# Kernel tuning notes

Hardware: AMD Instinct MI355X
Metric: run time of the kernel (lower is better)

Reference implementation:

```python
import jax, jax.numpy as jnp
import numpy as np

N_NODES = 50000
N_EDGES = 1600000
IN_CH = 128
HID_CH = 128


def setup_inputs() -> dict:
    key = jax.random.key(0)
    ks = jax.random.split(key, 8)
    node_embed = jax.random.normal(ks[0], (N_NODES, IN_CH), dtype=jnp.float32)
    node_pos = jax.random.normal(ks[1], (N_NODES, 3), dtype=jnp.float32)
    edge_index = jax.random.randint(ks[2], (2, N_EDGES), 0, N_NODES, dtype=jnp.int64)
    # Linear weights stored as [in, out] so y = x @ W + b (matches torch x @ W.T + b)
    W_res = jax.random.normal(ks[3], (IN_CH, HID_CH), dtype=jnp.float32) / np.sqrt(IN_CH)
    W_msg = jax.random.normal(ks[4], (2 * IN_CH + 1, HID_CH), dtype=jnp.float32) / np.sqrt(2 * IN_CH + 1)
    b_msg = jax.random.normal(ks[5], (HID_CH,), dtype=jnp.float32) * 0.01
    W_upd = jax.random.normal(ks[6], (IN_CH + HID_CH, HID_CH), dtype=jnp.float32) / np.sqrt(IN_CH + HID_CH)
    b_upd = jax.random.normal(ks[7], (HID_CH,), dtype=jnp.float32) * 0.01
    return {"node_embed": node_embed, "node_pos": node_pos, "edge_index": edge_index,
            "W_res": W_res, "W_msg": W_msg, "b_msg": b_msg, "W_upd": W_upd, "b_upd": b_upd}


def reference(node_embed, node_pos, edge_index, W_res, W_msg, b_msg, W_upd, b_upd):
    row, col = edge_index[0], edge_index[1]
    # squared distance per edge: [E, 1]
    diff = node_pos[row] - node_pos[col]
    dist = jnp.sum(diff * diff, axis=1, keepdims=True)
    # message MLP on concat(src, tgt, dist): [E, 2*in+1] -> [E, hidden]
    msg_in = jnp.concatenate([node_embed[row], node_embed[col], dist], axis=-1)
    msg = jax.nn.relu(msg_in @ W_msg + b_msg)
    # scatter-sum messages into target nodes (index = col, as in original)
    aggr = jax.ops.segment_sum(msg, col, num_segments=N_NODES)
    upd_in = jnp.concatenate([node_embed, aggr], axis=-1)
    new_node_embed = node_embed @ W_res + jax.nn.relu(upd_in @ W_upd + b_upd)
    return new_node_embed
```

## Files before the change

### kernel.cpp

```cpp
#include <hip/hip_runtime.h>
#include <hip/hip_bf16.h>
#include <cstdint>


typedef __bf16 bf16x8 __attribute__((ext_vector_type(8)));
typedef float floatx4 __attribute__((ext_vector_type(4)));
typedef float floatx2 __attribute__((ext_vector_type(2)));
typedef unsigned int uintx4 __attribute__((ext_vector_type(4)));

#define SBINS 128
#define SBIN_SHIFT 9
#define BIN_CAP 17408
#define CAP_OUT 19456
#define CUR_STRIDE 32

__device__ __forceinline__ ushort f2bf(float f) {
  union { float f; uint i; } v; v.f = f;
  uint r = v.i + 0x7fff + ((v.i >> 16) & 1);
  return (ushort)(r >> 16);
}
__device__ __forceinline__ bf16x8 load_frag(const ushort* p) {
  uint4 v = *(const uint4*)p;
  return __builtin_bit_cast(bf16x8, v);
}
__device__ __forceinline__ floatx2 pmax0(floatx2 a) {
#if __has_builtin(__builtin_elementwise_max)
  return __builtin_elementwise_max(a, (floatx2)(0.f));
#else
  floatx2 r; r.x = fmaxf(a.x, 0.f); r.y = fmaxf(a.y, 0.f); return r;
#endif
}
__device__ __forceinline__ floatx2 cvtpk2(uint qu) {
#if __has_builtin(__builtin_amdgcn_cvt_pk_f32_fp8)
  return __builtin_amdgcn_cvt_pk_f32_fp8((int)qu, false);
#else
  floatx2 o = {__builtin_amdgcn_cvt_f32_fp8((int)qu, 0),
               __builtin_amdgcn_cvt_f32_fp8((int)qu, 1)};
  return o;
#endif
}

struct WSrc { const float* s[5]; };

__global__ __launch_bounds__(256) void k01_cast_bin(
    const float* __restrict__ embed, ushort* __restrict__ Eb, int n4, int nb_cast,
    WSrc ws, ushort* __restrict__ Wt,
    const int* __restrict__ ei, int E,
    uint* __restrict__ bin_cursor, uint* __restrict__ binned, int bb)
{
  __shared__ uint hist[SBINS];
  __shared__ uint sbase[SBINS];
  __shared__ uint lcur[SBINS];

  if ((int)blockIdx.x >= bb) {
    int cb = blockIdx.x - bb;
    if (cb < nb_cast) {
      int i = cb * 256 + threadIdx.x;
      if (i < n4) {
        float4 v = ((const float4*)embed)[i];
        ushort4 o;
        o.x = f2bf(v.x); o.y = f2bf(v.y); o.z = f2bf(v.z); o.w = f2bf(v.w);
        ((ushort4*)Eb)[i] = o;
      }
      return;
    }
    int wb = cb - nb_cast;
    const float* s = ws.s[wb];
    ushort* d = Wt + wb * 16384;
    for (int i = threadIdx.x; i < 16384; i += 256) {
      int k = i >> 7, n = i & 127;
      d[n * 128 + k] = f2bf(s[i]);
    }
    return;
  }

  const int t = threadIdx.x;
  if (t < SBINS) hist[t] = 0;
  __syncthreads();

  const int e0 = blockIdx.x * 2048 + t * 8;
  int rr[8], cc[8];
  bool any = (e0 < E);
  if (any) {
    int4 r0 = ((const int4*)(ei + e0))[0];
    int4 r1 = ((const int4*)(ei + e0))[1];
    int4 c0 = ((const int4*)(ei + E + e0))[0];
    int4 c1 = ((const int4*)(ei + E + e0))[1];
    rr[0]=r0.x; rr[1]=r0.y; rr[2]=r0.z; rr[3]=r0.w;
    rr[4]=r1.x; rr[5]=r1.y; rr[6]=r1.z; rr[7]=r1.w;
    cc[0]=c0.x; cc[1]=c0.y; cc[2]=c0.z; cc[3]=c0.w;
    cc[4]=c1.x; cc[5]=c1.y; cc[6]=c1.z; cc[7]=c1.w;
#pragma unroll
    for (int j = 0; j < 8; ++j) {
      if (e0 + j < E) atomicAdd(&hist[cc[j] >> SBIN_SHIFT], 1u);
    }
  }
  __syncthreads();
  if (t < SBINS) {
    uint h = hist[t];
    sbase[t] = h ? atomicAdd(bin_cursor + t * CUR_STRIDE, h) : 0u;
    lcur[t] = 0;
  }
  __syncthreads();
  if (any) {
#pragma unroll
    for (int j = 0; j < 8; ++j) {
      if (e0 + j < E) {
        int b = cc[j] >> SBIN_SHIFT;
        uint ofs = atomicAdd(&lcur[b], 1u);
        uint idx = sbase[b] + ofs;
        if (idx < BIN_CAP)
          binned[(size_t)b * BIN_CAP + idx] = ((uint)cc[j] << 16) | (uint)rr[j];
      }
    }
  }
}

__global__ __launch_bounds__(256) void k2_proj_sort(
    const ushort* __restrict__ Ab, int M, int rt,
    const ushort* __restrict__ W1t, const ushort* __restrict__ W2t,
    const float* __restrict__ b_msg, const float* __restrict__ pos,
    unsigned char* __restrict__ P1, ushort* __restrict__ P2b,
    const uint* __restrict__ bin_cursor, const uint* __restrict__ binned,
    uint* __restrict__ sorted, int* __restrict__ nstart, int* __restrict__ ncnt)
{
  __shared__ uint  hist[512], st[512], lcur[512];
  __shared__ uint  part[256];
  __shared__ float spos[512 * 3];

  if ((int)blockIdx.x >= rt) {
    const int bin = blockIdx.x - rt;
    const int col0 = bin << SBIN_SHIFT;
    const int tid = threadIdx.x;
    const int cnt = (int)min(bin_cursor[bin * CUR_STRIDE], (uint)BIN_CAP);
    const uint* src = binned + (size_t)bin * BIN_CAP;
    const int ncol = min(512, M - col0);

    for (int i = tid; i < 512; i += 256) { hist[i] = 0; lcur[i] = 0; }
    for (int i = tid; i < ncol * 3; i += 256) spos[i] = pos[(size_t)col0 * 3 + i];
    __syncthreads();

    for (int i = tid; i < cnt; i += 256)
      atomicAdd(&hist[(src[i] >> 16) & 511u], 1u);
    __syncthreads();

    {
      uint a = hist[2 * tid], b = hist[2 * tid + 1];
      part[tid] = ((a + 3u) & ~3u) + ((b + 3u) & ~3u);
    }
    __syncthreads();
    if (tid == 0) {
      uint run = 0;
      for (int k = 0; k < 256; ++k) { uint tmp = part[k]; part[k] = run; run += tmp; }
    }
    __syncthreads();
    {
      uint a = hist[2 * tid];
      st[2 * tid] = part[tid];
      st[2 * tid + 1] = part[tid] + ((a + 3u) & ~3u);
    }
    __syncthreads();

    const size_t obase = (size_t)bin * CAP_OUT;
    int i = tid;
    for (; i + 1792 < cnt; i += 2048) {
      uint rc[8]; float dd[8];
#pragma unroll
      for (int j = 0; j < 8; ++j) rc[j] = src[i + j * 256];
#pragma unroll
      for (int j = 0; j < 8; ++j) {
        uint row = rc[j] & 0xffffu;
        uint cl  = (rc[j] >> 16) & 511u;
        float dx = spos[cl * 3 + 0] - pos[(size_t)row * 3 + 0];
        float dy = spos[cl * 3 + 1] - pos[(size_t)row * 3 + 1];
        float dz = spos[cl * 3 + 2] - pos[(size_t)row * 3 + 2];
        dd[j] = dx * dx + dy * dy + dz * dz;
      }
#pragma unroll
      for (int j = 0; j < 8; ++j) {
        uint cl = (rc[j] >> 16) & 511u;
        uint p = st[cl] + atomicAdd(&lcur[cl], 1u);
        sorted[obase + p] = (rc[j] << 16) | (uint)f2bf(dd[j]);
      }
    }
    for (; i < cnt; i += 256) {
      uint rc = src[i];
      uint row = rc & 0xffffu;
      uint cl  = (rc >> 16) & 511u;
      float dx = spos[cl * 3 + 0] - pos[(size_t)row * 3 + 0];
      float dy = spos[cl * 3 + 1] - pos[(size_t)row * 3 + 1];
      float dz = spos[cl * 3 + 2] - pos[(size_t)row * 3 + 2];
      float d = dx * dx + dy * dy + dz * dz;
      uint p = st[cl] + atomicAdd(&lcur[cl], 1u);
      sorted[obase + p] = (rc << 16) | (uint)f2bf(d);
    }
    __syncthreads();

    for (int c = tid; c < ncol; c += 256) {
      nstart[col0 + c] = (int)(obase + st[c]);
      ncnt[col0 + c] = (int)hist[c];
    }
    return;
  }

  const int wv = threadIdx.x >> 6, lane = threadIdx.x & 63;
  const int q = lane >> 4, lr = lane & 15;
  const int m0 = blockIdx.x * 32;
  const int n0 = wv * 32;

  const ushort* Wt2[2] = {W1t, W2t};
  bf16x8 bfr[2][2][4];
#pragma unroll
  for (int ws = 0; ws < 2; ++ws)
#pragma unroll
    for (int nt = 0; nt < 2; ++nt) {
      int colc = n0 + nt * 16 + lr;
#pragma unroll
      for (int kc = 0; kc < 4; ++kc)
        bfr[ws][nt][kc] = load_frag(Wt2[ws] + colc * 128 + kc * 32 + q * 8);
    }

  floatx4 z = {0.f, 0.f, 0.f, 0.f};
  floatx4 acc[2][2][2];
#pragma unroll
  for (int ws = 0; ws < 2; ++ws)
#pragma unroll
    for (int mt = 0; mt < 2; ++mt)
#pragma unroll
      for (int nt = 0; nt < 2; ++nt) acc[ws][mt][nt] = z;

  const int r0 = min(m0 + lr, M - 1);
  const int r1 = min(m0 + 16 + lr, M - 1);
#pragma unroll
  for (int kc = 0; kc < 4; ++kc) {
    bf16x8 a0 = load_frag(Ab + (size_t)r0 * 128 + kc * 32 + q * 8);
    bf16x8 a1 = load_frag(Ab + (size_t)r1 * 128 + kc * 32 + q * 8);
#pragma unroll
    for (int ws = 0; ws < 2; ++ws)
#pragma unroll
      for (int nt = 0; nt < 2; ++nt) {
        acc[ws][0][nt] = __builtin_amdgcn_mfma_f32_16x16x32_bf16(a0, bfr[ws][nt][kc], acc[ws][0][nt], 0, 0, 0);
        acc[ws][1][nt] = __builtin_amdgcn_mfma_f32_16x16x32_bf16(a1, bfr[ws][nt][kc], acc[ws][1][nt], 0, 0, 0);
      }
  }

#pragma unroll
  for (int nt = 0; nt < 2; ++nt) {
    int colc = n0 + nt * 16 + lr;
    float bias = b_msg[colc];
#pragma unroll
    for (int mt = 0; mt < 2; ++mt)
#pragma unroll
      for (int i = 0; i < 4; ++i) {
        int r = m0 + mt * 16 + q * 4 + i;
        if (r < M) {
          int p8 = __builtin_amdgcn_cvt_pk_fp8_f32(acc[0][mt][nt][i], 0.f, 0, false);
          P1[(size_t)r * 128 + colc] = (unsigned char)(p8 & 0xff);
          P2b[(size_t)r * 128 + colc] = f2bf(acc[1][mt][nt][i] + bias);
        }
      }
  }
}

__global__ __launch_bounds__(256) void aggregate(const int* __restrict__ ncnt,
                                                 const int* __restrict__ nstart,
                                                 const uint* __restrict__ sorted,
                                                 const unsigned char* __restrict__ P1,
                                                 const ushort* __restrict__ P2b,
                                                 const float* __restrict__ wd,
                                                 ushort* __restrict__ aggr, int M)
{
  const int lane = threadIdx.x & 63;
  const int ch = lane * 2;
  const int wid = blockIdx.x * 4 + (threadIdx.x >> 6);
  const int nw = gridDim.x * 4;

  float2 wl = *(const float2*)(wd + ch);
  floatx2 wv = {wl.x, wl.y};

  for (int n = wid; n < M; n += nw) {
    uint p2u = *(const uint*)(P2b + (size_t)n * 128 + ch);
    floatx2 p2 = {__int_as_float((int)(p2u << 16)),
                  __int_as_float((int)(p2u & 0xffff0000u))};

    const int cnt = ncnt[n];
    const uint* base = sorted + nstart[n];

    floatx2 accA = {0.f, 0.f}, accB = {0.f, 0.f};

    auto edge = [&](uint rec, floatx2& acc) {
      float d = __int_as_float((int)(rec << 16));
      uint off = ((rec >> 9) & 0x007fff80u) | (uint)ch;
      uint qu = (uint)*(const ushort*)(P1 + off);
#if __has_builtin(__builtin_elementwise_fma)
      floatx2 u = __builtin_elementwise_fma((floatx2)(d), wv, p2);
#else
      floatx2 u = (floatx2)(d) * wv + p2;
#endif
      floatx2 t = cvtpk2(qu) + u;
      acc += pmax0(t);
    };

    int i = 0;
    for (; i + 8 <= cnt; i += 8) {
      uintx4 ra = __builtin_nontemporal_load((const uintx4*)(base + i));
      uintx4 rb = __builtin_nontemporal_load((const uintx4*)(base + i + 4));
      edge(ra.x, accA); edge(ra.y, accB); edge(ra.z, accA); edge(ra.w, accB);
      edge(rb.x, accA); edge(rb.y, accB); edge(rb.z, accA); edge(rb.w, accB);
    }
    for (; i < cnt; ++i) edge(base[i], accA);

    floatx2 acc = accA + accB;
    uint o = (uint)f2bf(acc.x) | ((uint)f2bf(acc.y) << 16);
    *(uint*)(aggr + (size_t)n * 128 + ch) = o;
  }
}

__global__ __launch_bounds__(256) void gemm_upd_mfma(
    const ushort* __restrict__ Eb, const ushort* __restrict__ Gb, int M,
    const ushort* __restrict__ Wu1t, const ushort* __restrict__ Wu2t,
    const ushort* __restrict__ Wrt, const float* __restrict__ b_upd,
    float* __restrict__ out)
{
  const int wv = threadIdx.x >> 6, lane = threadIdx.x & 63;
  const int q = lane >> 4, lr = lane & 15;
  const int m0 = blockIdx.x * 32;
  const int n0 = wv * 32;

  bf16x8 b1[2][4], b2[2][4], br[2][4];
#pragma unroll
  for (int nt = 0; nt < 2; ++nt) {
    int colc = n0 + nt * 16 + lr;
#pragma unroll
    for (int kc = 0; kc < 4; ++kc) {
      b1[nt][kc] = load_frag(Wu1t + colc * 128 + kc * 32 + q * 8);
      b2[nt][kc] = load_frag(Wu2t + colc * 128 + kc * 32 + q * 8);
      br[nt][kc] = load_frag(Wrt  + colc * 128 + kc * 32 + q * 8);
    }
  }

  floatx4 z = {0.f, 0.f, 0.f, 0.f};
  floatx4 acc_u[2][2], acc_r[2][2];
#pragma unroll
  for (int mt = 0; mt < 2; ++mt)
#pragma unroll
    for (int nt = 0; nt < 2; ++nt) { acc_u[mt][nt] = z; acc_r[mt][nt] = z; }

  const int r0 = min(m0 + lr, M - 1);
  const int r1 = min(m0 + 16 + lr, M - 1);
#pragma unroll
  for (int kc = 0; kc < 4; ++kc) {
    bf16x8 ae0 = load_frag(Eb + (size_t)r0 * 128 + kc * 32 + q * 8);
    bf16x8 ae1 = load_frag(Eb + (size_t)r1 * 128 + kc * 32 + q * 8);
    bf16x8 ag0 = load_frag(Gb + (size_t)r0 * 128 + kc * 32 + q * 8);
    bf16x8 ag1 = load_frag(Gb + (size_t)r1 * 128 + kc * 32 + q * 8);
#pragma unroll
    for (int nt = 0; nt < 2; ++nt) {
      acc_u[0][nt] = __builtin_amdgcn_mfma_f32_16x16x32_bf16(ae0, b1[nt][kc], acc_u[0][nt], 0, 0, 0);
      acc_u[1][nt] = __builtin_amdgcn_mfma_f32_16x16x32_bf16(ae1, b1[nt][kc], acc_u[1][nt], 0, 0, 0);
      acc_u[0][nt] = __builtin_amdgcn_mfma_f32_16x16x32_bf16(ag0, b2[nt][kc], acc_u[0][nt], 0, 0, 0);
      acc_u[1][nt] = __builtin_amdgcn_mfma_f32_16x16x32_bf16(ag1, b2[nt][kc], acc_u[1][nt], 0, 0, 0);
      acc_r[0][nt] = __builtin_amdgcn_mfma_f32_16x16x32_bf16(ae0, br[nt][kc], acc_r[0][nt], 0, 0, 0);
      acc_r[1][nt] = __builtin_amdgcn_mfma_f32_16x16x32_bf16(ae1, br[nt][kc], acc_r[1][nt], 0, 0, 0);
    }
  }

#pragma unroll
  for (int nt = 0; nt < 2; ++nt) {
    int colc = n0 + nt * 16 + lr;
    float bias = b_upd[colc];
#pragma unroll
    for (int mt = 0; mt < 2; ++mt)
#pragma unroll
      for (int i = 0; i < 4; ++i) {
        int r = m0 + mt * 16 + q * 4 + i;
        if (r < M)
          out[(size_t)r * 128 + colc] = acc_r[mt][nt][i] + fmaxf(acc_u[mt][nt][i] + bias, 0.f);
      }
  }
}

extern "C" void kernel_launch(void* const* d_in, const int* in_sizes, int n_in,
                              void* d_out, int out_size, void* d_ws, size_t ws_size,
                              hipStream_t stream)
{
  const float* embed = (const float*)d_in[0];
  const float* pos   = (const float*)d_in[1];
  const int*   ei    = (const int*)d_in[2];
  const float* W_res = (const float*)d_in[3];
  const float* W_msg = (const float*)d_in[4];
  const float* b_msg = (const float*)d_in[5];
  const float* W_upd = (const float*)d_in[6];
  const float* b_upd = (const float*)d_in[7];
  float* out = (float*)d_out;

  const int M = in_sizes[0] / 128;
  const int E = in_sizes[2] / 2;

  ushort* Eb = (ushort*)d_ws;
  unsigned char* P1f8 = (unsigned char*)(Eb + (size_t)M * 128);
  ushort* P2b = (ushort*)(P1f8 + (size_t)M * 128);
  ushort* Gb  = P2b + (size_t)M * 128;
  ushort* Wt  = Gb  + (size_t)M * 128;
  uint*   binned = (uint*)(Wt + 5 * 16384);
  uint*   sorted = binned + (size_t)SBINS * BIN_CAP;
  int*    nstart = (int*)(sorted + (size_t)SBINS * CAP_OUT);
  int*    ncnt   = nstart + M;
  uint*   bin_cursor = (uint*)(ncnt + M);

  (void)hipMemsetAsync(bin_cursor, 0, (size_t)SBINS * CUR_STRIDE * sizeof(uint), stream);

  WSrc wsrc;
  wsrc.s[0] = W_msg;
  wsrc.s[1] = W_msg + 128 * 128;
  wsrc.s[2] = W_res;
  wsrc.s[3] = W_upd;
  wsrc.s[4] = W_upd + 128 * 128;

  int n4 = M * 128 / 4;
  int nb_cast = (n4 + 255) / 256;
  int bb = (E + 2047) / 2048;
  k01_cast_bin<<<bb + nb_cast + 5, 256, 0, stream>>>(
      embed, Eb, n4, nb_cast, wsrc, Wt, ei, E, bin_cursor, binned, bb);

  int rt = (M + 31) / 32;
  int nsb = (M + 511) >> SBIN_SHIFT;
  k2_proj_sort<<<rt + nsb, 256, 0, stream>>>(
      Eb, M, rt, Wt, Wt + 16384, b_msg, pos, P1f8, P2b,
      bin_cursor, binned, sorted, nstart, ncnt);

  int ab = min((M + 3) / 4, 2048);
  aggregate<<<ab, 256, 0, stream>>>(ncnt, nstart, sorted, P1f8, P2b,
                                    W_msg + 256 * 128, Gb, M);

  gemm_upd_mfma<<<rt, 256, 0, stream>>>(Eb, Gb, M, Wt + 3 * 16384, Wt + 4 * 16384,
                                        Wt + 2 * 16384, b_upd, out);
}
```

Before: 278.2 us.

## Split per-bin counting sort into eight sub-bin blocks staged in shared memory

The sort phase of the projection kernel now runs eight blocks per 512-column bin, each handling a 64-column sub-range. Each block scans the whole bin but keeps only its own columns, scatters them into a shared-memory buffer, then writes that buffer out contiguously. This replaces random global scatter writes with coalesced stores and gives the GPU more, smaller blocks. Sort blocks are also moved ahead of the GEMM blocks in the grid so they start first. In exchange every bin's input is read eight times, and the fixed per-sub-bin capacity could overflow and silently drop edges.

```diff
diff --git a/kernel.cpp b/kernel.cpp
--- a/kernel.cpp
+++ b/kernel.cpp
@@ -11,7 +11,8 @@
 #define SBINS 128
 #define SBIN_SHIFT 9
 #define BIN_CAP 17408
-#define CAP_OUT 19456
+#define SUB_CAP 2560
+#define SUB_STRIDE 2816
 #define CUR_STRIDE 32
 
 __device__ __forceinline__ ushort f2bf(float f) {
@@ -117,95 +118,73 @@
 }
 
 __global__ __launch_bounds__(256) void k2_proj_sort(
-    const ushort* __restrict__ Ab, int M, int rt,
+    const ushort* __restrict__ Ab, int M, int nst,
     const ushort* __restrict__ W1t, const ushort* __restrict__ W2t,
     const float* __restrict__ b_msg, const float* __restrict__ pos,
     unsigned char* __restrict__ P1, ushort* __restrict__ P2b,
     const uint* __restrict__ bin_cursor, const uint* __restrict__ binned,
     uint* __restrict__ sorted, int* __restrict__ nstart, int* __restrict__ ncnt)
 {
-  __shared__ uint  hist[512], st[512], lcur[512];
-  __shared__ uint  part[256];
-  __shared__ float spos[512 * 3];
-
-  if ((int)blockIdx.x >= rt) {
-    const int bin = blockIdx.x - rt;
-    const int col0 = bin << SBIN_SHIFT;
+  __shared__ uint  srt[SUB_STRIDE];
+  __shared__ float spos[64 * 3];
+  __shared__ uint  h64[64], st64[64], lc64[64];
+  __shared__ uint  stot;
+
+  if ((int)blockIdx.x < nst) {
+    const int u = blockIdx.x;
+    const int bin = u >> 3, s = u & 7;
+    const int col0 = (bin << SBIN_SHIFT) + (s << 6);
+    if (col0 >= M) return;
+    const int ncol = min(64, M - col0);
     const int tid = threadIdx.x;
     const int cnt = (int)min(bin_cursor[bin * CUR_STRIDE], (uint)BIN_CAP);
     const uint* src = binned + (size_t)bin * BIN_CAP;
-    const int ncol = min(512, M - col0);
-
-    for (int i = tid; i < 512; i += 256) { hist[i] = 0; lcur[i] = 0; }
+
+    if (tid < 64) { h64[tid] = 0; lc64[tid] = 0; }
     for (int i = tid; i < ncol * 3; i += 256) spos[i] = pos[(size_t)col0 * 3 + i];
     __syncthreads();
 
-    for (int i = tid; i < cnt; i += 256)
-      atomicAdd(&hist[(src[i] >> 16) & 511u], 1u);
+    for (int i = tid; i < cnt; i += 256) {
+      uint cl = (src[i] >> 16) & 511u;
+      if ((int)(cl >> 6) == s) atomicAdd(&h64[cl & 63u], 1u);
+    }
     __syncthreads();
 
-    {
-      uint a = hist[2 * tid], b = hist[2 * tid + 1];
-      part[tid] = ((a + 3u) & ~3u) + ((b + 3u) & ~3u);
-    }
-    __syncthreads();
     if (tid == 0) {
       uint run = 0;
-      for (int k = 0; k < 256; ++k) { uint tmp = part[k]; part[k] = run; run += tmp; }
+      for (int c = 0; c < 64; ++c) { st64[c] = run; run += (h64[c] + 3u) & ~3u; }
+      stot = min(run, (uint)SUB_STRIDE);
     }
     __syncthreads();
-    {
-      uint a = hist[2 * tid];
-      st[2 * tid] = part[tid];
-      st[2 * tid + 1] = part[tid] + ((a + 3u) & ~3u);
+
+    for (int i = tid; i < cnt; i += 256) {
+      uint rc = src[i];
+      uint cl = (rc >> 16) & 511u;
+      if ((int)(cl >> 6) == s) {
+        uint row = rc & 0xffffu, c6 = cl & 63u;
+        float dx = spos[c6 * 3 + 0] - pos[(size_t)row * 3 + 0];
+        float dy = spos[c6 * 3 + 1] - pos[(size_t)row * 3 + 1];
+        float dz = spos[c6 * 3 + 2] - pos[(size_t)row * 3 + 2];
+        float d = dx * dx + dy * dy + dz * dz;
+        uint p = st64[c6] + atomicAdd(&lc64[c6], 1u);
+        if (p < SUB_STRIDE) srt[p] = (row << 16) | (uint)f2bf(d);
+      }
     }
     __syncthreads();
 
-    const size_t obase = (size_t)bin * CAP_OUT;
-    int i = tid;
-    for (; i + 1792 < cnt; i += 2048) {
-      uint rc[8]; float dd[8];
-#pragma unroll
-      for (int j = 0; j < 8; ++j) rc[j] = src[i + j * 256];
-#pragma unroll
-      for (int j = 0; j < 8; ++j) {
-        uint row = rc[j] & 0xffffu;
-        uint cl  = (rc[j] >> 16) & 511u;
-        float dx = spos[cl * 3 + 0] - pos[(size_t)row * 3 + 0];
-        float dy = spos[cl * 3 + 1] - pos[(size_t)row * 3 + 1];
-        float dz = spos[cl * 3 + 2] - pos[(size_t)row * 3 + 2];
-        dd[j] = dx * dx + dy * dy + dz * dz;
-      }
-#pragma unroll
-      for (int j = 0; j < 8; ++j) {
-        uint cl = (rc[j] >> 16) & 511u;
-        uint p = st[cl] + atomicAdd(&lcur[cl], 1u);
-        sorted[obase + p] = (rc[j] << 16) | (uint)f2bf(dd[j]);
-      }
-    }
-    for (; i < cnt; i += 256) {
-      uint rc = src[i];
-      uint row = rc & 0xffffu;
-      uint cl  = (rc >> 16) & 511u;
-      float dx = spos[cl * 3 + 0] - pos[(size_t)row * 3 + 0];
-      float dy = spos[cl * 3 + 1] - pos[(size_t)row * 3 + 1];
-      float dz = spos[cl * 3 + 2] - pos[(size_t)row * 3 + 2];
-      float d = dx * dx + dy * dy + dz * dz;
-      uint p = st[cl] + atomicAdd(&lcur[cl], 1u);
-      sorted[obase + p] = (rc << 16) | (uint)f2bf(d);
-    }
-    __syncthreads();
-
-    for (int c = tid; c < ncol; c += 256) {
-      nstart[col0 + c] = (int)(obase + st[c]);
-      ncnt[col0 + c] = (int)hist[c];
+    const size_t obase = (size_t)(bin * 8 + s) * SUB_STRIDE;
+    for (int i = tid; i < (int)stot; i += 256)
+      sorted[obase + i] = srt[i];
+    if (tid < ncol) {
+      nstart[col0 + tid] = (int)(obase + st64[tid]);
+      ncnt[col0 + tid] = (int)h64[tid];
     }
     return;
   }
 
   const int wv = threadIdx.x >> 6, lane = threadIdx.x & 63;
   const int q = lane >> 4, lr = lane & 15;
-  const int m0 = blockIdx.x * 32;
+  const int m0 = (blockIdx.x - nst) * 32;
   const int n0 = wv * 32;
 
   const ushort* Wt2[2] = {W1t, W2t};
@@ -404,7 +383,7 @@
   ushort* Wt  = Gb  + (size_t)M * 128;
   uint*   binned = (uint*)(Wt + 5 * 16384);
   uint*   sorted = binned + (size_t)SBINS * BIN_CAP;
-  int*    nstart = (int*)(sorted + (size_t)SBINS * CAP_OUT);
+  int*    nstart = (int*)(sorted + (size_t)SBINS * 8 * SUB_STRIDE);
   int*    ncnt   = nstart + M;
   uint*   bin_cursor = (uint*)(ncnt + M);
 
@@ -425,8 +404,9 @@
 
   int rt = (M + 31) / 32;
   int nsb = (M + 511) >> SBIN_SHIFT;
-  k2_proj_sort<<<rt + nsb, 256, 0, stream>>>(
-      Eb, M, rt, Wt, Wt + 16384, b_msg, pos, P1f8, P2b,
+  int nst = nsb * 8;
+  k2_proj_sort<<<nst + rt, 256, 0, stream>>>(
+      Eb, M, nst, Wt, Wt + 16384, b_msg, pos, P1f8, P2b,
       bin_cursor, binned, sorted, nstart, ncnt);
 
   int ab = min((M + 3) / 4, 2048);
```

Measured after the change: 295.0 us. 1.06x slower.
